# Kernel optimization log

Hardware: AMD Instinct MI355X
Metric: run time of the kernel (lower is better)

Reference implementation:

```python
import jax, jax.numpy as jnp
import numpy as np

KS = 3          # kernel_size
DIM = 3         # dimension
B, N = 4, 16384
CMAX = 64       # voxel coordinate range [0, CMAX)
K = KS ** DIM   # kernel_volume = 27
SHIFT = KS      # makes neighbor coords non-negative
BASE = CMAX + 2 * KS  # per-axis encoding base


def _kernel_offsets():
    # matches torch: arange(-ks//2 + 1, ks//2 + 1) per dim, meshgrid 'ij'
    r = jnp.arange(-(KS) // 2 + 1, KS // 2 + 1)
    grid = jnp.meshgrid(*([r] * DIM), indexing='ij')
    return jnp.stack(grid, axis=-1).reshape(-1, DIM)  # [K, DIM]


def setup_inputs() -> dict:
    key = jax.random.key(0)
    k1, _ = jax.random.split(key)
    coordinates = jax.random.randint(k1, (B, N, DIM), 0, CMAX, dtype=jnp.int32)
    batch_indices = jnp.broadcast_to(jnp.arange(B, dtype=jnp.int32)[:, None], (B, N))
    return {"coordinates": coordinates, "batch_indices": batch_indices}


def reference(coordinates, batch_indices):
    """Vectorized kernel-map construction (replaces the Python dict-hash loops).

    Returns:
      in_idx  [B*N*K] : index of the input point within its batch
      out_idx [B*N*K] : dense output index (first-appearance order, matches dict insertion)
      rel_pos [B*N*K] : kernel offset index
      out_key [B*N*K, 3] : unique output coordinates, padded with -1 past num_out
      num_out [] : number of valid unique output keys
    """
    Bv, Nv, D = coordinates.shape
    offsets = _kernel_offsets()            # [K, 3]
    Kv = offsets.shape[0]
    # neighbor coordinates, iteration order (b, idx, k) == torch loop order
    nb = coordinates[:, :, None, :] + offsets[None, None, :, :]  # [B, N, K, 3]
    c = nb + SHIFT                                               # non-negative
    b_ids = batch_indices[:, :, None].astype(jnp.int32)
    keys = (b_ids * (BASE ** 3)
            + (c[..., 0] * BASE + c[..., 1]) * BASE + c[..., 2]).reshape(-1)  # [T]
    T = keys.shape[0]
    sentinel = jnp.int32(Bv * (BASE ** 3))  # > any real key
    uniq, first_idx, inv = jnp.unique(keys, size=T, fill_value=sentinel,
                                      return_index=True, return_inverse=True)
    valid = uniq != sentinel
    # recover first-appearance (dict-insertion) order from sorted-unique
    first_adj = jnp.where(valid, first_idx, T)
    order = jnp.argsort(first_adj)                      # insertion order -> sorted pos
    rank = jnp.zeros((T,), dtype=jnp.int32).at[order].set(jnp.arange(T, dtype=jnp.int32))
    out_idx = rank[inv]                                 # [T] dense output indices
    # decode unique keys back to (x, y, z) in insertion order
    uo = uniq[order]
    vo = valid[order]
    rem = uo % (BASE ** 3)
    x = rem // (BASE * BASE) - SHIFT
    y = (rem // BASE) % BASE - SHIFT
    z = rem % BASE - SHIFT
    out_key = jnp.where(vo[:, None], jnp.stack([x, y, z], axis=-1), -1)  # [T, 3]
    num_out = vo.sum()
    in_idx = jnp.tile(jnp.repeat(jnp.arange(Nv, dtype=jnp.int32), Kv), Bv)
    rel_pos = jnp.tile(jnp.arange(Kv, dtype=jnp.int32), Bv * Nv)
    return in_idx, out_idx, rel_pos, out_key, num_out
```

## Files before the change

### kernel.cpp

```cpp
#include <hip/hip_runtime.h>

namespace {
constexpr int Bc   = 4;
constexpr int Nc   = 16384;
constexpr int Kc   = 27;
constexpr int Pc   = 68;
constexpr int P2c  = Pc * Pc;
constexpr int P3c  = Pc * P2c;
constexpr int NPts = Bc * Nc;
constexpr int Tc   = NPts * Kc;
constexpr int FT   = Bc * P3c;
constexpr unsigned INFu = 0xFFFFFFFFu;
constexpr int PLANES = Bc * Pc;
constexpr int SLABS  = 4;
constexpr int SROWS  = 17;
constexpr int PBLKS  = 1024;
constexpr int PPTS   = NPts / PBLKS;
constexpr int OBLKS  = 864;
constexpr int OCHUNK = 8;
}

__device__ __forceinline__ unsigned min3u(unsigned a, unsigned b, unsigned c) {
    return min(min(a, b), c);
}

__global__ void __launch_bounds__(256)
k1_atomic_easy(const int* __restrict__ coords, const int* __restrict__ batch,
               unsigned* __restrict__ cm, unsigned* __restrict__ pcoord,
               int* __restrict__ in_idx, int* __restrict__ rel_pos) {
    const int g = blockIdx.x * 256 + threadIdx.x;
    if (g < NPts) {
        const int bb = batch[g];
        const int x = coords[3 * g], y = coords[3 * g + 1], z = coords[3 * g + 2];
        pcoord[g] = (unsigned)(x | (y << 6) | (z << 12) | (bb << 18));
        atomicMin(&cm[bb * P3c + (x + 2) * P2c + (y + 2) * Pc + (z + 2)],
                  (unsigned)(g & (Nc - 1)));
    }
    const int t = 4 * g;
    int4 a, r;
    a.x = (t / Kc) & (Nc - 1);       r.x = t % Kc;
    a.y = ((t + 1) / Kc) & (Nc - 1); r.y = (t + 1) % Kc;
    a.z = ((t + 2) / Kc) & (Nc - 1); r.z = (t + 2) % Kc;
    a.w = ((t + 3) / Kc) & (Nc - 1); r.w = (t + 3) % Kc;
    reinterpret_cast<int4*>(in_idx)[g]  = a;
    reinterpret_cast<int4*>(rel_pos)[g] = r;
}

__global__ void __launch_bounds__(256)
k2_planes(const unsigned* __restrict__ cm, unsigned* __restrict__ Btab) {
    __shared__ unsigned s0[(SROWS + 2) * Pc];
    __shared__ unsigned s1[(SROWS + 2) * Pc];
    const int tid  = threadIdx.x;
    const int p    = blockIdx.x / SLABS;
    const int slab = blockIdx.x - p * SLABS;
    const int r0   = slab * SROWS;
    const int base = p * P2c;

    const int n4 = (SROWS + 2) * Pc / 4;
    for (int i4 = tid; i4 < n4; i4 += 256) {
        const int li  = 4 * i4;
        const int row = r0 - 1 + li / Pc;
        uint4 v = make_uint4(INFu, INFu, INFu, INFu);
        if (row >= 0 && row < Pc)
            v = reinterpret_cast<const uint4*>(cm + base + row * Pc)[i4 % (Pc / 4)];
        reinterpret_cast<uint4*>(s0)[i4] = v;
    }
    __syncthreads();
    for (int i = tid; i < (SROWS + 2) * Pc; i += 256) {
        const int col = i % Pc;
        unsigned v = INFu;
        if (col >= 1 && col <= 66) v = min3u(s0[i - 1], s0[i], s0[i + 1]);
        s1[i] = v;
    }
    __syncthreads();
    for (int i = tid; i < SROWS * Pc; i += 256) {
        const int lr  = i / Pc;
        const int col = i - lr * Pc;
        const int row = r0 + lr;
        unsigned v = INFu;
        if (row >= 1 && row <= 66) {
            const int li = (lr + 1) * Pc + col;
            v = min3u(s1[li - Pc], s1[li], s1[li + Pc]);
        }
        Btab[base + row * Pc + col] = v;
    }
}

__global__ void __launch_bounds__(256)
k3_pred(const unsigned* __restrict__ pcoord, const unsigned* __restrict__ Btab,
        unsigned short* __restrict__ owners,
        unsigned long long* __restrict__ packed, int* __restrict__ blockSums) {
    __shared__ int parts[PPTS][4];
    __shared__ int pbs[PPTS];
    __shared__ int scn[256];
    const int tid = threadIdx.x, bid = blockIdx.x;
    const int p = tid >> 2, j = tid & 3;
    const int pt = bid * PPTS + p;

    int mypb = 0;
    if (j < 3) {
        const unsigned pc = pcoord[pt];
        const int x = pc & 63, y = (pc >> 6) & 63, z = (pc >> 12) & 63,
                  bb = pc >> 18;
        const unsigned uidx = (unsigned)(pt & (Nc - 1));
        const unsigned* basep =
            Btab + bb * P3c + (x * Pc + (y + j + 1)) * Pc + (z + 1);
        unsigned w[5][3];
        #pragma unroll
        for (int xi = 0; xi < 5; ++xi) {
            const unsigned* q = basep + xi * P2c;
            w[xi][0] = q[0]; w[xi][1] = q[1]; w[xi][2] = q[2];
        }
        #pragma unroll
        for (int dxl = 0; dxl < 3; ++dxl)
            #pragma unroll
            for (int dz = 0; dz < 3; ++dz) {
                const unsigned m = min3u(w[dxl][dz], w[dxl + 1][dz],
                                         w[dxl + 2][dz]);
                const int kk = (dxl * 3 + j) * 3 + dz;
                owners[pt * Kc + kk] = (unsigned short)m;
                mypb |= (m == uidx) ? (1 << kk) : 0;
            }
    }
    parts[p][j] = mypb;
    __syncthreads();
    if (j == 0) pbs[p] = parts[p][0] | parts[p][1] | parts[p][2];
    __syncthreads();

    const int v = (tid < PPTS) ? __popc(pbs[tid]) : 0;
    scn[tid] = v;
    __syncthreads();
    #pragma unroll
    for (int off = 1; off < PPTS; off <<= 1) {
        int u = (tid >= off) ? scn[tid - off] : 0;
        __syncthreads();
        scn[tid] += u;
        __syncthreads();
    }
    if (tid < PPTS) {
        const int intra = scn[tid] - v;
        packed[bid * PPTS + tid] =
            (unsigned long long)(unsigned)pbs[tid]
          | ((unsigned long long)(unsigned)intra << 27)
          | ((unsigned long long)pcoord[bid * PPTS + tid] << 38);
    }
    if (tid == PPTS - 1) blockSums[bid] = scn[PPTS - 1];
}

__global__ void __launch_bounds__(256)
k4_outputs(const unsigned short* __restrict__ owners,
           const unsigned long long* __restrict__ packed,
           const int* __restrict__ blockSums,
           int* __restrict__ out_idx, int* __restrict__ out_key,
           int* __restrict__ num_out) {
    __shared__ int pref[PBLKS];
    __shared__ int scn[256];
    __shared__ int s_total;
    const int tid = threadIdx.x, bid = blockIdx.x;

    const int4 bsv = reinterpret_cast<const int4*>(blockSums)[tid];
    const int s = bsv.x + bsv.y + bsv.z + bsv.w;
    scn[tid] = s;
    __syncthreads();
    #pragma unroll
    for (int off = 1; off < 256; off <<= 1) {
        int u = (tid >= off) ? scn[tid - off] : 0;
        __syncthreads();
        scn[tid] += u;
        __syncthreads();
    }
    const int excl = scn[tid] - s;
    pref[4 * tid + 0] = excl;
    pref[4 * tid + 1] = excl + bsv.x;
    pref[4 * tid + 2] = excl + bsv.x + bsv.y;
    pref[4 * tid + 3] = excl + bsv.x + bsv.y + bsv.z;
    if (tid == 255) s_total = scn[255];
    __syncthreads();

    const int total = s_total;
    const int t0 = bid * (256 * OCHUNK) + tid;

    int oo[OCHUNK];
    #pragma unroll
    for (int c = 0; c < OCHUNK; ++c) oo[c] = (int)owners[t0 + c * 256];

    int pts[OCHUNK], ks[OCHUNK];
    unsigned long long pw[OCHUNK], po[OCHUNK];
    #pragma unroll
    for (int c = 0; c < OCHUNK; ++c) {
        const int t  = t0 + c * 256;
        const int pt = t / Kc;
        pts[c] = pt;
        ks[c]  = t - Kc * pt;
        pw[c]  = packed[pt];
        po[c]  = packed[(pt & ~(Nc - 1)) | oo[c]];
    }

    #pragma unroll
    for (int c = 0; c < OCHUNK; ++c) {
        const int t  = t0 + c * 256;
        const int pt = pts[c];
        const int k  = ks[c];
        const unsigned long long pkw = pw[c];
        const int pbw    = (int)(pkw & 0x7ffffffull);
        const int intraw = (int)((pkw >> 27) & 0x7ffull);
        const unsigned pcw = (unsigned)(pkw >> 38);
        const int x = pcw & 63, y = (pcw >> 6) & 63, z = (pcw >> 12) & 63;
        const int dx = k / 9 - 1;
        const int dy = (k / 3) % 3 - 1;
        const int dz = k - (k / 3) * 3 - 1;
        const int cx = x + dx, cy = y + dy, cz = z + dz;

        const unsigned long long pko = po[c];
        const int pbo    = (int)(pko & 0x7ffffffull);
        const int intrao = (int)((pko >> 27) & 0x7ffull);
        const unsigned pco = (unsigned)(pko >> 38);
        const int ox = pco & 63, oy = (pco >> 6) & 63, oz = (pco >> 12) & 63;
        const int kp = (cx - ox + 1) * 9 + (cy - oy + 1) * 3 + (cz - oz + 1);
        const int go = (pt & ~(Nc - 1)) | oo[c];
        out_idx[t] = pref[go >> 6] + intrao + __popc(pbo & ((1 << kp) - 1));

        if ((pbw >> k) & 1) {
            const int r = pref[pt >> 6] + intraw + __popc(pbw & ((1 << k) - 1));
            out_key[3 * r + 0] = cx;
            out_key[3 * r + 1] = cy;
            out_key[3 * r + 2] = cz;
        }
        if (t >= total) {
            out_key[3 * t + 0] = -1;
            out_key[3 * t + 1] = -1;
            out_key[3 * t + 2] = -1;
        }
        if (t == 0) num_out[0] = total;
    }
}

extern "C" void kernel_launch(void* const* d_in, const int* in_sizes, int n_in,
                              void* d_out, int out_size, void* d_ws, size_t ws_size,
                              hipStream_t stream) {
    const int* coords = (const int*)d_in[0];
    const int* batch  = (const int*)d_in[1];
    int* out = (int*)d_out;
    int* in_idx  = out;
    int* out_idx = out + Tc;
    int* rel_pos = out + 2 * Tc;
    int* out_key = out + 3 * Tc;
    int* num_out = out + 6 * Tc;

    unsigned* ws = (unsigned*)d_ws;
    unsigned* cm   = ws;
    unsigned* Btab = ws + FT;
    unsigned long long* packed =
        (unsigned long long*)(ws + 2 * FT);
    unsigned short* owners =
        (unsigned short*)(packed + NPts);
    int* blockSums = (int*)(owners + Tc);
    unsigned* pcoord = (unsigned*)(blockSums + PBLKS);

    k1_atomic_easy<<<Tc / 4 / 256, 256, 0, stream>>>(coords, batch, cm, pcoord,
                                                     in_idx, rel_pos);
    k2_planes<<<PLANES * SLABS, 256, 0, stream>>>(cm, Btab);
    k3_pred<<<PBLKS, 256, 0, stream>>>(pcoord, Btab, owners, packed, blockSums);
    k4_outputs<<<OBLKS, 256, 0, stream>>>(owners, packed, blockSums,
                                          out_idx, out_key, num_out);
}
```

Measured before the change: 98.56 us.

## Assign contiguous 8-element runs per thread with vectorized owner loads and stores

Each thread in the final output kernel now handles eight consecutive output slots instead of eight slots strided by the block size. Owners are read as one 16-byte vector of packed 16-bit values, out_idx is written with two int4 stores, and the -1 padding of out_key uses six int4 stores. The owning-point lookups drop to two per thread, and the per-element divide by 27 becomes an incremental counter. The cost is that adjacent threads now touch addresses 32 bytes apart, so global accesses are less coalesced. The code also assumes owners are stored as 16-bit values and that the pointers are 16-byte aligned.

```diff
diff --git a/kernel.cpp b/kernel.cpp
--- a/kernel.cpp
+++ b/kernel.cpp
@@ -17,7 +17,6 @@
 constexpr int PBLKS  = 1024;
 constexpr int PPTS   = NPts / PBLKS;
 constexpr int OBLKS  = 864;
-constexpr int OCHUNK = 8;
 }
 
 __device__ __forceinline__ unsigned min3u(unsigned a, unsigned b, unsigned c) {
@@ -178,61 +177,83 @@
     __syncthreads();
 
     const int total = s_total;
-    const int t0 = bid * (256 * OCHUNK) + tid;
-
-    int oo[OCHUNK];
-    #pragma unroll
-    for (int c = 0; c < OCHUNK; ++c) oo[c] = (int)owners[t0 + c * 256];
-
-    int pts[OCHUNK], ks[OCHUNK];
-    unsigned long long pw[OCHUNK], po[OCHUNK];
-    #pragma unroll
-    for (int c = 0; c < OCHUNK; ++c) {
-        const int t  = t0 + c * 256;
-        const int pt = t / Kc;
-        pts[c] = pt;
-        ks[c]  = t - Kc * pt;
-        pw[c]  = packed[pt];
-        po[c]  = packed[(pt & ~(Nc - 1)) | oo[c]];
-    }
-
-    #pragma unroll
-    for (int c = 0; c < OCHUNK; ++c) {
-        const int t  = t0 + c * 256;
-        const int pt = pts[c];
-        const int k  = ks[c];
-        const unsigned long long pkw = pw[c];
-        const int pbw    = (int)(pkw & 0x7ffffffull);
-        const int intraw = (int)((pkw >> 27) & 0x7ffull);
-        const unsigned pcw = (unsigned)(pkw >> 38);
-        const int x = pcw & 63, y = (pcw >> 6) & 63, z = (pcw >> 12) & 63;
-        const int dx = k / 9 - 1;
-        const int dy = (k / 3) % 3 - 1;
-        const int dz = k - (k / 3) * 3 - 1;
-        const int cx = x + dx, cy = y + dy, cz = z + dz;
-
-        const unsigned long long pko = po[c];
-        const int pbo    = (int)(pko & 0x7ffffffull);
-        const int intrao = (int)((pko >> 27) & 0x7ffull);
-        const unsigned pco = (unsigned)(pko >> 38);
-        const int ox = pco & 63, oy = (pco >> 6) & 63, oz = (pco >> 12) & 63;
-        const int kp = (cx - ox + 1) * 9 + (cy - oy + 1) * 3 + (cz - oz + 1);
-        const int go = (pt & ~(Nc - 1)) | oo[c];
-        out_idx[t] = pref[go >> 6] + intrao + __popc(pbo & ((1 << kp) - 1));
-
-        if ((pbw >> k) & 1) {
-            const int r = pref[pt >> 6] + intraw + __popc(pbw & ((1 << k) - 1));
-            out_key[3 * r + 0] = cx;
-            out_key[3 * r + 1] = cy;
-            out_key[3 * r + 2] = cz;
-        }
-        if (t >= total) {
+    const int g  = bid * 256 + tid;
+    const int t0 = g * 8;
+
+    const uint4 owv = reinterpret_cast<const uint4*>(owners)[g];
+    int oo[8];
+    oo[0] = owv.x & 0xffff; oo[1] = owv.x >> 16;
+    oo[2] = owv.y & 0xffff; oo[3] = owv.y >> 16;
+    oo[4] = owv.z & 0xffff; oo[5] = owv.z >> 16;
+    oo[6] = owv.w & 0xffff; oo[7] = owv.w >> 16;
+
+    const int pt0 = t0 / Kc;
+    const int pt1 = (t0 + 7) / Kc;
+    const unsigned long long pw0 = packed[pt0];
+    const unsigned long long pw1 = packed[pt1];
+
+    unsigned long long po[8];
+    {
+        int pt = pt0, kk = t0 - Kc * pt0;
+        #pragma unroll
+        for (int c = 0; c < 8; ++c) {
+            po[c] = packed[(pt & ~(Nc - 1)) | oo[c]];
+            if (++kk == Kc) { kk = 0; ++pt; }
+        }
+    }
+
+    int outv[8];
+    {
+        int pt = pt0, kk = t0 - Kc * pt0;
+        #pragma unroll
+        for (int c = 0; c < 8; ++c) {
+            const int t = t0 + c;
+            const unsigned long long pkw = (pt == pt0) ? pw0 : pw1;
+            const int pbw    = (int)(pkw & 0x7ffffffull);
+            const int intraw = (int)((pkw >> 27) & 0x7ffull);
+            const unsigned pcw = (unsigned)(pkw >> 38);
+            const int x = pcw & 63, y = (pcw >> 6) & 63, z = (pcw >> 12) & 63;
+            const int dx = kk / 9 - 1;
+            const int dy = (kk / 3) % 3 - 1;
+            const int dz = kk - (kk / 3) * 3 - 1;
+            const int cx = x + dx, cy = y + dy, cz = z + dz;
+
+            const unsigned long long pko = po[c];
+            const int pbo    = (int)(pko & 0x7ffffffull);
+            const int intrao = (int)((pko >> 27) & 0x7ffull);
+            const unsigned pco = (unsigned)(pko >> 38);
+            const int ox = pco & 63, oy = (pco >> 6) & 63, oz = (pco >> 12) & 63;
+            const int kp = (cx - ox + 1) * 9 + (cy - oy + 1) * 3 + (cz - oz + 1);
+            const int go = (pt & ~(Nc - 1)) | oo[c];
+            outv[c] = pref[go >> 6] + intrao + __popc(pbo & ((1 << kp) - 1));
+
+            if ((pbw >> kk) & 1) {
+                const int r = pref[pt >> 6] + intraw
+                            + __popc(pbw & ((1 << kk) - 1));
+                out_key[3 * r + 0] = cx;
+                out_key[3 * r + 1] = cy;
+                out_key[3 * r + 2] = cz;
+            }
+            if (++kk == Kc) { kk = 0; ++pt; }
+        }
+    }
+    int4* o4 = reinterpret_cast<int4*>(out_idx + t0);
+    o4[0] = make_int4(outv[0], outv[1], outv[2], outv[3]);
+    o4[1] = make_int4(outv[4], outv[5], outv[6], outv[7]);
+
+    if (t0 >= total) {
+        int4* k4p = reinterpret_cast<int4*>(out_key + 3 * t0);
+        const int4 m1 = make_int4(-1, -1, -1, -1);
+        #pragma unroll
+        for (int i = 0; i < 6; ++i) k4p[i] = m1;
+    } else if (t0 + 7 >= total) {
+        for (int t = total; t < t0 + 8; ++t) {
             out_key[3 * t + 0] = -1;
             out_key[3 * t + 1] = -1;
             out_key[3 * t + 2] = -1;
         }
-        if (t == 0) num_out[0] = total;
-    }
+    }
+    if (g == 0) num_out[0] = total;
 }
 
 extern "C" void kernel_launch(void* const* d_in, const int* in_sizes, int n_in,
```

Measured after the change: 104.3 us. 1.06x slower.
